# Kernel tuning notes

Hardware: AMD Instinct MI355X
Metric: run time of the kernel (lower is better)

## Reference

```python
import jax, jax.numpy as jnp
import numpy as np

IN_FEATURES = 2048
N_CLASSES = 10000
BATCH = 8192


def setup_inputs() -> dict:
    key = jax.random.key(0)
    kx, ka, kb, kbias = jax.random.split(key, 4)
    x = jax.random.normal(kx, (BATCH, IN_FEATURES), dtype=jnp.float32)
    # kaiming_normal_ with nonlinearity='relu': std = sqrt(2 / fan_in)
    # A: (n_classes, 1) -> fan_in = 1; B: (1, in_features) -> fan_in = in_features
    A = jax.random.normal(ka, (N_CLASSES, 1), dtype=jnp.float32) * np.sqrt(2.0 / 1.0)
    B = jax.random.normal(kb, (1, IN_FEATURES), dtype=jnp.float32) * np.sqrt(2.0 / IN_FEATURES)
    bias = jax.random.normal(kbias, (N_CLASSES,), dtype=jnp.float32)
    return {"x": x, "A": A, "B": B, "bias": bias}


def reference(x, A, B, bias):
    # Original: out = relu(x @ (A @ B)^T + bias)
    # Reassociated rank-1 form: s = x @ B^T  -> [batch, 1]; out = s @ A^T + bias
    s = x @ B.T                      # [batch, 1]
    out = s * A[:, 0][None, :] + bias  # [batch, n_classes]
    return jax.nn.relu(out)
```

## Files before the change

kernel.cpp:

```cpp
#include <hip/hip_runtime.h>


#define BATCH       8192
#define IN_FEATURES 2048
#define N_CLASSES   10000
#define NC4         2500
#define NF4         512
#define BLOCK       256
#define K2_ROWS     32

typedef float fx4 __attribute__((ext_vector_type(4)));

__global__ __launch_bounds__(BLOCK) void lora_dot_wave_kernel(
    const float* __restrict__ x,
    const float* __restrict__ B,
    float* __restrict__ s_out)
{
    const int lane = threadIdx.x & 63;
    const int wid  = threadIdx.x >> 6;
    const int row  = blockIdx.x * 4 + wid;

    const fx4* __restrict__ xr = reinterpret_cast<const fx4*>(x + (size_t)row * IN_FEATURES);
    const fx4* __restrict__ B4 = reinterpret_cast<const fx4*>(B);

    float acc = 0.0f;
    #pragma unroll
    for (int k = 0; k < NF4 / 64; ++k) {
        fx4 xv = __builtin_nontemporal_load(&xr[lane + 64 * k]);
        fx4 bv = B4[lane + 64 * k];
        acc = fmaf(xv.x, bv.x, acc);
        acc = fmaf(xv.y, bv.y, acc);
        acc = fmaf(xv.z, bv.z, acc);
        acc = fmaf(xv.w, bv.w, acc);
    }

    #pragma unroll
    for (int off = 32; off > 0; off >>= 1)
        acc += __shfl_down(acc, off, 64);

    if (lane == 0) s_out[row] = acc;
}

__global__ __launch_bounds__(BLOCK) void lora_store_kernel(
    const float* __restrict__ s_vec,
    const float* __restrict__ A,
    const float* __restrict__ bias,
    float* __restrict__ out)
{
    const int tid  = threadIdx.x;
    const int col4 = blockIdx.x * BLOCK + tid;
    const int row0 = blockIdx.y * K2_ROWS;

    __shared__ float s_lds[K2_ROWS];
    if (tid < K2_ROWS) s_lds[tid] = s_vec[row0 + tid];
    __syncthreads();

    if (col4 >= NC4) return;

    const fx4 a = reinterpret_cast<const fx4*>(A)[col4];
    const fx4 b = reinterpret_cast<const fx4*>(bias)[col4];

    fx4* __restrict__ o = reinterpret_cast<fx4*>(out) + (size_t)row0 * NC4 + col4;

    #pragma unroll
    for (int r = 0; r < K2_ROWS; ++r) {
        const float s = s_lds[r];
        fx4 v;
        v.x = fmaxf(fmaf(s, a.x, b.x), 0.0f);
        v.y = fmaxf(fmaf(s, a.y, b.y), 0.0f);
        v.z = fmaxf(fmaf(s, a.z, b.z), 0.0f);
        v.w = fmaxf(fmaf(s, a.w, b.w), 0.0f);
        __builtin_nontemporal_store(v, &o[(size_t)r * NC4]);
    }
}

extern "C" void kernel_launch(void* const* d_in, const int* in_sizes, int n_in,
                              void* d_out, int out_size, void* d_ws, size_t ws_size,
                              hipStream_t stream) {
    const float* x    = (const float*)d_in[0];
    const float* A    = (const float*)d_in[1];
    const float* B    = (const float*)d_in[2];
    const float* bias = (const float*)d_in[3];
    float* out        = (float*)d_out;
    float* s_vec      = (float*)d_ws;

    lora_dot_wave_kernel<<<BATCH / 4, BLOCK, 0, stream>>>(x, B, s_vec);

    dim3 grid((NC4 + BLOCK - 1) / BLOCK, BATCH / K2_ROWS);
    lora_store_kernel<<<grid, BLOCK, 0, stream>>>(s_vec, A, bias, out);
}
```

Before: 77.72 us.

## Fuse dot-product and broadcast store into one wave-per-row kernel

New measurement: 86.36 us. +11.1%, slower.

```diff
diff --git a/kernel.cpp b/kernel.cpp
--- a/kernel.cpp
+++ b/kernel.cpp
@@ -5,27 +5,29 @@
 #define IN_FEATURES 2048
 #define N_CLASSES   10000
 #define NC4         2500
-#define NF4         512
 #define BLOCK       256
-#define K2_ROWS     32
+#define WPB         4
+#define GRID        (BATCH / WPB)
 
 typedef float fx4 __attribute__((ext_vector_type(4)));
 
-__global__ __launch_bounds__(BLOCK) void lora_dot_wave_kernel(
+__global__ __launch_bounds__(BLOCK, 8) void lora_waverow_kernel(
     const float* __restrict__ x,
+    const float* __restrict__ A,
     const float* __restrict__ B,
-    float* __restrict__ s_out)
+    const float* __restrict__ bias,
+    float* __restrict__ out)
 {
     const int lane = threadIdx.x & 63;
     const int wid  = threadIdx.x >> 6;
-    const int row  = blockIdx.x * 4 + wid;
+    const int row  = blockIdx.x * WPB + wid;
 
     const fx4* __restrict__ xr = reinterpret_cast<const fx4*>(x + (size_t)row * IN_FEATURES);
     const fx4* __restrict__ B4 = reinterpret_cast<const fx4*>(B);
 
     float acc = 0.0f;
     #pragma unroll
-    for (int k = 0; k < NF4 / 64; ++k) {
+    for (int k = 0; k < 8; ++k) {
         fx4 xv = __builtin_nontemporal_load(&xr[lane + 64 * k]);
         fx4 bv = B4[lane + 64 * k];
         acc = fmaf(xv.x, bv.x, acc);
@@ -36,41 +38,22 @@
 
     #pragma unroll
     for (int off = 32; off > 0; off >>= 1)
-        acc += __shfl_down(acc, off, 64);
+        acc += __shfl_xor(acc, off, 64);
+    const float s = acc;
 
-    if (lane == 0) s_out[row] = acc;
-}
+    const fx4* __restrict__ A4  = reinterpret_cast<const fx4*>(A);
+    const fx4* __restrict__ bb4 = reinterpret_cast<const fx4*>(bias);
+    fx4* __restrict__ o = reinterpret_cast<fx4*>(out) + (size_t)row * NC4;
 
-__global__ __launch_bounds__(BLOCK) void lora_store_kernel(
-    const float* __restrict__ s_vec,
-    const float* __restrict__ A,
-    const float* __restrict__ bias,
-    float* __restrict__ out)
-{
-    const int tid  = threadIdx.x;
-    const int col4 = blockIdx.x * BLOCK + tid;
-    const int row0 = blockIdx.y * K2_ROWS;
-
-    __shared__ float s_lds[K2_ROWS];
-    if (tid < K2_ROWS) s_lds[tid] = s_vec[row0 + tid];
-    __syncthreads();
-
-    if (col4 >= NC4) return;
-
-    const fx4 a = reinterpret_cast<const fx4*>(A)[col4];
-    const fx4 b = reinterpret_cast<const fx4*>(bias)[col4];
-
-    fx4* __restrict__ o = reinterpret_cast<fx4*>(out) + (size_t)row0 * NC4 + col4;
-
-    #pragma unroll
-    for (int r = 0; r < K2_ROWS; ++r) {
-        const float s = s_lds[r];
+    for (int j = lane; j < NC4; j += 64) {
+        fx4 a = A4[j];
+        fx4 b = bb4[j];
         fx4 v;
         v.x = fmaxf(fmaf(s, a.x, b.x), 0.0f);
         v.y = fmaxf(fmaf(s, a.y, b.y), 0.0f);
         v.z = fmaxf(fmaf(s, a.z, b.z), 0.0f);
         v.w = fmaxf(fmaf(s, a.w, b.w), 0.0f);
-        __builtin_nontemporal_store(v, &o[(size_t)r * NC4]);
+        __builtin_nontemporal_store(v, &o[j]);
     }
 }
 
@@ -82,10 +65,6 @@
     const float* B    = (const float*)d_in[2];
     const float* bias = (const float*)d_in[3];
     float* out        = (float*)d_out;
-    float* s_vec      = (float*)d_ws;
 
-    lora_dot_wave_kernel<<<BATCH / 4, BLOCK, 0, stream>>>(x, B, s_vec);
-
-    dim3 grid((NC4 + BLOCK - 1) / BLOCK, BATCH / K2_ROWS);
-    lora_store_kernel<<<grid, BLOCK, 0, stream>>>(s_vec, A, bias, out);
+    lora_waverow_kernel<<<GRID, BLOCK, 0, stream>>>(x, A, B, bias, out);
 }
```
